# Kernel optimization log

Hardware: AMD Instinct MI355X
Metric: run time of the kernel (lower is better)

The kernel has to match this reference:

```python
import jax, jax.numpy as jnp
import numpy as np

# Swin block config (matches init_kwargs)
DIM = 192
HEADS = 6
HEAD_DIM = 32
INNER = HEADS * HEAD_DIM  # 192
MLP = 768
WS = 7                    # window size
DISP = WS // 2            # cyclic shift displacement = 3
NEG = -1e9                # stands in for -inf in the shift masks
EPS = 1e-5


def setup_inputs() -> dict:
    key = jax.random.key(0)
    ks = jax.random.split(key, 8)
    B, H, W = 8, 112, 112
    x = jax.random.normal(ks[0], (B, H, W, DIM), dtype=jnp.float32)
    w_qkv = jax.random.normal(ks[1], (DIM, 3 * INNER), dtype=jnp.float32) * 0.02
    w_out = jax.random.normal(ks[2], (INNER, DIM), dtype=jnp.float32) * 0.02
    b_out = jnp.zeros((DIM,), jnp.float32)
    pos_emb = jax.random.normal(ks[3], (2 * WS - 1, 2 * WS - 1), dtype=jnp.float32)
    ln1_g = jnp.ones((DIM,), jnp.float32)
    ln1_b = jnp.zeros((DIM,), jnp.float32)
    ln2_g = jnp.ones((DIM,), jnp.float32)
    ln2_b = jnp.zeros((DIM,), jnp.float32)
    w1 = jax.random.normal(ks[4], (DIM, MLP), dtype=jnp.float32) * 0.02
    b1 = jnp.zeros((MLP,), jnp.float32)
    w2 = jax.random.normal(ks[5], (MLP, DIM), dtype=jnp.float32) * 0.02
    b2 = jnp.zeros((DIM,), jnp.float32)
    return {"x": x, "w_qkv": w_qkv, "w_out": w_out, "b_out": b_out,
            "pos_emb": pos_emb, "ln1_g": ln1_g, "ln1_b": ln1_b,
            "ln2_g": ln2_g, "ln2_b": ln2_b,
            "w1": w1, "b1": b1, "w2": w2, "b2": b2}


def _layernorm(x, g, b):
    mu = jnp.mean(x, axis=-1, keepdims=True)
    var = jnp.var(x, axis=-1, keepdims=True)
    return (x - mu) * jax.lax.rsqrt(var + EPS) * g + b


def _rel_bias(pos_emb):
    # relative position bias, gathered to (ws^2, ws^2)
    coords = jnp.stack(jnp.meshgrid(jnp.arange(WS), jnp.arange(WS), indexing="ij"), -1).reshape(-1, 2)
    rel = coords[:, None, :] - coords[None, :, :] + WS - 1  # in [0, 2*WS-2]
    return pos_emb[rel[..., 0], rel[..., 1]]


def _shift_masks(nw_h, nw_w):
    ws2 = WS * WS
    ul = jnp.zeros((ws2, ws2), jnp.float32)
    ul = ul.at[-DISP * WS:, :-DISP * WS].set(NEG)
    ul = ul.at[:-DISP * WS, -DISP * WS:].set(NEG)
    lr = jnp.zeros((WS, WS, WS, WS), jnp.float32)
    lr = lr.at[:, -DISP:, :, :-DISP].set(NEG)
    lr = lr.at[:, :-DISP:, :, -DISP:].set(NEG)
    lr = lr.reshape(ws2, ws2)
    full = jnp.zeros((nw_h * nw_w, ws2, ws2), jnp.float32)
    full = full.at[-nw_w:].add(ul)            # bottom row of windows
    full = full.at[nw_w - 1::nw_w].add(lr)    # rightmost column of windows
    return full


def _window_attention(x, w_qkv, w_out, b_out, pos_emb):
    x = jnp.roll(x, (-DISP, -DISP), axis=(1, 2))  # cyclic shift
    B, H, W, _ = x.shape
    nw_h, nw_w = H // WS, W // WS
    ws2 = WS * WS
    qkv = x @ w_qkv  # (B,H,W,3*INNER)
    qkv = qkv.reshape(B, nw_h, WS, nw_w, WS, 3, HEADS, HEAD_DIM)
    # -> (3, B, heads, n_windows, ws^2, head_dim)
    qkv = qkv.transpose(5, 0, 6, 1, 3, 2, 4, 7).reshape(3, B, HEADS, nw_h * nw_w, ws2, HEAD_DIM)
    q, k, v = qkv[0], qkv[1], qkv[2]
    dots = jnp.einsum("bhwid,bhwjd->bhwij", q, k) * (HEAD_DIM ** -0.5)
    dots = dots + _rel_bias(pos_emb)                       # (ws2,ws2) broadcast
    dots = dots + _shift_masks(nw_h, nw_w)                 # (nw,ws2,ws2) broadcast
    attn = jax.nn.softmax(dots, axis=-1)
    out = jnp.einsum("bhwij,bhwjd->bhwid", attn, v)
    # merge windows back: (B, nw_h, WS, nw_w, WS, heads*head_dim)
    out = out.reshape(B, HEADS, nw_h, nw_w, WS, WS, HEAD_DIM)
    out = out.transpose(0, 2, 4, 3, 5, 1, 6).reshape(B, H, W, INNER)
    out = out @ w_out + b_out
    return jnp.roll(out, (DISP, DISP), axis=(1, 2))  # cyclic back-shift


def reference(x, w_qkv, w_out, b_out, pos_emb, ln1_g, ln1_b, ln2_g, ln2_b, w1, b1, w2, b2):
    # Residual(PreNorm(WindowAttention))
    x = x + _window_attention(_layernorm(x, ln1_g, ln1_b), w_qkv, w_out, b_out, pos_emb)
    # Residual(PreNorm(FeedForward))  with exact (erf) GELU as in nn.GELU
    h = _layernorm(x, ln2_g, ln2_b)
    h = jax.nn.gelu(h @ w1 + b1, approximate=False) @ w2 + b2
    return x + h
```

## Files before the change

kernel.cpp:

```cpp
#include <hip/hip_runtime.h>
#include <hip/hip_bf16.h>
#include <math.h>

typedef __hip_bfloat16 bf16;
typedef unsigned short ushort_t;
typedef __bf16 bf16x8 __attribute__((ext_vector_type(8)));
typedef unsigned short ushortx8 __attribute__((ext_vector_type(8)));
typedef float  f32x4  __attribute__((ext_vector_type(4)));

#define BATCH 8
#define HH 112
#define WW 112
#define CDIM 192
#define HEADS 6
#define HD 32
#define QKVW 576
#define MLPW 768
#define WS 7
#define WS2 49
#define NWH 16
#define NWW 16
#define NWIN 256
#define NTOK (BATCH*HH*WW)
#define NEGV (-1e9f)

typedef __attribute__((address_space(3))) void lds_void;
typedef const __attribute__((address_space(1))) void gbl_void;

__device__ __forceinline__ float toF(float v) { return v; }
__device__ __forceinline__ float toF(bf16 v) { return __bfloat162float(v); }
__device__ __forceinline__ bf16  f2b(float v) { return __float2bfloat16(v); }
__device__ __forceinline__ ushort_t f2u(float v) { bf16 b = __float2bfloat16(v); return *(ushort_t*)&b; }

__device__ __forceinline__ bool probe_is_bf16(const void* p) {
    const unsigned int* w = (const unsigned int*)p;
    int nz = 0, band = 0;
    #pragma unroll
    for (int i = 0; i < 16; i++) {
        unsigned int v = w[i];
        if (v == 0u) continue;
        nz++;
        unsigned int lo = v & 0xFFFFu, hi = v >> 16;
        unsigned int elo = (lo >> 7) & 0xFFu, ehi = (hi >> 7) & 0xFFu;
        bool okl = (lo != 0u) && (elo >= 0x60u) && (elo <= 0x9Fu);
        bool okh = (hi != 0u) && (ehi >= 0x60u) && (ehi <= 0x9Fu);
        if (okl && okh) band++;
    }
    return (nz == 0) || (band == nz);
}

__device__ __forceinline__ float read_any(const void* p, size_t i, bool isb) {
    return isb ? toF(((const bf16*)p)[i]) : ((const float*)p)[i];
}

__device__ __forceinline__ float wave_sum(float v) {
    #pragma unroll
    for (int o = 1; o < 64; o <<= 1) v += __shfl_xor(v, o, 64);
    return v;
}

__global__ void canon_kernel(const void* __restrict__ src, float* __restrict__ dst, int n) {
    bool isb = probe_is_bf16(src);
    int i = blockIdx.x * 256 + threadIdx.x;
    if (i < n) dst[i] = read_any(src, i, isb);
}

__global__ void canon_bt_kernel(const void* __restrict__ src, ushort_t* __restrict__ dstT,
                                int K, int N) {
    bool isb = probe_is_bf16(src);
    int i = blockIdx.x * 256 + threadIdx.x;
    if (i < K * N) {
        int k = i / N, n = i % N;
        dstT[(size_t)n * K + k] = f2u(read_any(src, i, isb));
    }
}

__global__ void ln1_kernel(const void* __restrict__ xraw, const float* __restrict__ g,
                           const float* __restrict__ bta, bf16* __restrict__ out) {
    bool xb = probe_is_bf16(xraw);
    int wave = threadIdx.x >> 6, lane = threadIdx.x & 63;
    int t = blockIdx.x * 4 + wave;
    size_t base = (size_t)t * CDIM;
    float v[3];
    #pragma unroll
    for (int i = 0; i < 3; i++) v[i] = read_any(xraw, base + lane + 64 * i, xb);
    float s  = v[0] + v[1] + v[2];
    float s2 = v[0]*v[0] + v[1]*v[1] + v[2]*v[2];
    s = wave_sum(s); s2 = wave_sum(s2);
    float mu = s * (1.0f / CDIM);
    float var = s2 * (1.0f / CDIM) - mu * mu;
    float rs = rsqrtf(var + 1e-5f);
    #pragma unroll
    for (int i = 0; i < 3; i++) {
        int c = lane + 64 * i;
        out[base + c] = f2b((v[i] - mu) * rs * g[c] + bta[c]);
    }
}

template <int EPI, int NY>
__global__ __launch_bounds__(256) void gemm_kernel(
    const ushort_t* __restrict__ A, const ushort_t* __restrict__ BT,
    const int K, const int N,
    const float* __restrict__ bias,
    const void* __restrict__ res,
    void* __restrict__ out)
{
    __shared__ ushort_t As[2][128 * 64];
    __shared__ ushort_t Bs[2][64 * 64];
    int tid = threadIdx.x;
    int per = gridDim.x >> 3;
    int sid = blockIdx.x;
    int w = (sid & 7) * per + (sid >> 3);
    int t0 = (w / NY) * 128;
    int n0 = (w % NY) * 64;
    int lane = tid & 63, wv = tid >> 6;
    int l15 = lane & 15, quad = lane >> 4;
    int lr = lane >> 3;
    int lc = lane & 7;

    f32x4 acc[2][4];
    #pragma unroll
    for (int i = 0; i < 2; i++)
        #pragma unroll
        for (int j = 0; j < 4; j++)
            acc[i][j] = (f32x4){0.f, 0.f, 0.f, 0.f};

    auto stage = [&](int kb, int buf) {
        #pragma unroll
        for (int it = 0; it < 4; it++) {
            int r = wv * 32 + it * 8 + lr;
            const ushort_t* src = &A[(size_t)(t0 + r) * K + kb + ((lc ^ (r & 7)) << 3)];
            __builtin_amdgcn_global_load_lds(
                (gbl_void*)src, (lds_void*)&As[buf][(wv * 32 + it * 8) * 64], 16, 0, 0);
        }
        #pragma unroll
        for (int it = 0; it < 2; it++) {
            int r = wv * 16 + it * 8 + lr;
            const ushort_t* src = &BT[(size_t)(n0 + r) * K + kb + ((lc ^ (r & 7)) << 3)];
            __builtin_amdgcn_global_load_lds(
                (gbl_void*)src, (lds_void*)&Bs[buf][(wv * 16 + it * 8) * 64], 16, 0, 0);
        }
    };

    const int nkb = K >> 6;
    stage(0, 0);
    __syncthreads();

    for (int t = 0; t < nkb; t++) {
        int cur = t & 1;
        if (t + 1 < nkb) stage((t + 1) << 6, cur ^ 1);
        #pragma unroll
        for (int kk = 0; kk < 64; kk += 32) {
            int cs = (((kk >> 3) + quad) ^ (l15 & 7)) << 3;
            bf16x8 af[2], bfr[4];
            #pragma unroll
            for (int i = 0; i < 2; i++)
                af[i] = *(const bf16x8*)(&As[cur][(wv * 32 + i * 16 + l15) * 64 + cs]);
            #pragma unroll
            for (int j = 0; j < 4; j++)
                bfr[j] = *(const bf16x8*)(&Bs[cur][(j * 16 + l15) * 64 + cs]);
            #pragma unroll
            for (int i = 0; i < 2; i++)
                #pragma unroll
                for (int j = 0; j < 4; j++)
                    acc[i][j] = __builtin_amdgcn_mfma_f32_16x16x32_bf16(af[i], bfr[j], acc[i][j], 0, 0, 0);
        }
        __syncthreads();
    }

    bool xb = false;
    if (EPI == 1) xb = probe_is_bf16(res);

    #pragma unroll
    for (int i = 0; i < 2; i++) {
        #pragma unroll
        for (int j = 0; j < 4; j++) {
            #pragma unroll
            for (int r = 0; r < 4; r++) {
                int row = wv * 32 + i * 16 + quad * 4 + r;
                int col = n0 + j * 16 + l15;
                size_t t = (size_t)(t0 + row);
                float v = acc[i][j][r];
                if (EPI == 0) {
                    ((bf16*)out)[t * N + col] = f2b(v);
                } else {
                    size_t o = t * CDIM + col;
                    ((bf16*)out)[o] = f2b(v + bias[col] + read_any(res, o, xb));
                }
            }
        }
    }
}

__global__ __launch_bounds__(256, 2) void fused_mlp_kernel(
    const bf16* __restrict__ X,
    const ushort_t* __restrict__ W1T,
    const ushort_t* __restrict__ W2T,
    const float* __restrict__ g, const float* __restrict__ bta,
    const float* __restrict__ b1, const float* __restrict__ b2,
    float* __restrict__ out)
{
    __shared__ ushort_t W1s[3 * 64 * 64];
    __shared__ ushort_t W2s[192 * 64];
    __shared__ ushort_t Hs[128 * 64];
    int tid = threadIdx.x;
    int lane = tid & 63, wv = tid >> 6;
    int l15 = lane & 15, quad = lane >> 4;
    int lr = lane >> 3, lc = lane & 7;
    int t0 = blockIdx.x * 128;

    auto stageW1 = [&](int c) {
        #pragma unroll
        for (int p = 0; p < 3; p++)
            #pragma unroll
            for (int rg = 0; rg < 2; rg++) {
                int rowb = wv * 16 + rg * 8;
                const ushort_t* src =
                    &W1T[(size_t)(c * 64 + rowb + lr) * CDIM + p * 64 + ((lc ^ lr) << 3)];
                __builtin_amdgcn_global_load_lds(
                    (gbl_void*)src, (lds_void*)&W1s[p * 4096 + rowb * 64], 16, 0, 0);
            }
    };
    auto stageW2 = [&](int c) {
        #pragma unroll
        for (int rg = 0; rg < 6; rg++) {
            int rowb = wv * 48 + rg * 8;
            const ushort_t* src =
                &W2T[(size_t)(rowb + lr) * MLPW + c * 64 + ((lc ^ lr) << 3)];
            __builtin_amdgcn_global_load_lds(
                (gbl_void*)src, (lds_void*)&W2s[rowb * 64], 16, 0, 0);
        }
    };

    stageW1(0);
    stageW2(0);

    bf16x8 af[2][6];
    float s[2] = {0.f, 0.f}, s2[2] = {0.f, 0.f};
    #pragma unroll
    for (int m = 0; m < 2; m++) {
        size_t rb = (size_t)(t0 + wv * 32 + m * 16 + l15) * CDIM;
        #pragma unroll
        for (int kk = 0; kk < 6; kk++) {
            af[m][kk] = *(const bf16x8*)((const ushort_t*)X + rb + kk * 32 + quad * 8);
            #pragma unroll
            for (int j = 0; j < 8; j++) {
                float f = (float)af[m][kk][j];
                s[m] += f; s2[m] += f * f;
            }
        }
    }
    #pragma unroll
    for (int m = 0; m < 2; m++) {
        s[m]  += __shfl_xor(s[m], 16, 64);  s[m]  += __shfl_xor(s[m], 32, 64);
        s2[m] += __shfl_xor(s2[m], 16, 64); s2[m] += __shfl_xor(s2[m], 32, 64);
    }
    #pragma unroll
    for (int kk = 0; kk < 6; kk++) {
        int c0 = kk * 32 + quad * 8;
        float4 g0 = *(const float4*)(g + c0), g1 = *(const float4*)(g + c0 + 4);
        float4 b0 = *(const float4*)(bta + c0), b1v = *(const float4*)(bta + c0 + 4);
        const float* gp[2] = {&g0.x, &g1.x};
        const float* bp[2] = {&b0.x, &b1v.x};
        #pragma unroll
        for (int m = 0; m < 2; m++) {
            float mu = s[m] * (1.0f / CDIM);
            float var = s2[m] * (1.0f / CDIM) - mu * mu;
            float rs = rsqrtf(var + 1e-5f);
            #pragma unroll
            for (int j = 0; j < 8; j++)
                af[m][kk][j] = (__bf16)(((float)af[m][kk][j] - mu) * rs * gp[j >> 2][j & 3]
                                        + bp[j >> 2][j & 3]);
        }
    }

    f32x4 acc2[2][12];
    #pragma unroll
    for (int m = 0; m < 2; m++)
        #pragma unroll
        for (int nt = 0; nt < 12; nt++) acc2[m][nt] = (f32x4){0.f, 0.f, 0.f, 0.f};

    __syncthreads();

    for (int c = 0; c < 12; c++) {
        f32x4 hacc[2][4];
        #pragma unroll
        for (int m = 0; m < 2; m++)
            #pragma unroll
            for (int nt = 0; nt < 4; nt++) hacc[m][nt] = (f32x4){0.f, 0.f, 0.f, 0.f};
        #pragma unroll
        for (int kk = 0; kk < 6; kk++) {
            int p = kk >> 1;
            int cc = (kk & 1) * 4 + quad;
            #pragma unroll
            for (int nt = 0; nt < 4; nt++) {
                int n = nt * 16 + l15;
                bf16x8 bfr = *(const bf16x8*)(&W1s[p * 4096 + n * 64 + ((cc ^ (n & 7)) << 3)]);
                #pragma unroll
                for (int m = 0; m < 2; m++)
                    hacc[m][nt] = __builtin_amdgcn_mfma_f32_16x16x32_bf16(af[m][kk], bfr, hacc[m][nt], 0, 0, 0);
            }
        }
        float b1v[4];
        #pragma unroll
        for (int nt = 0; nt < 4; nt++) b1v[nt] = b1[c * 64 + nt * 16 + l15];
        #pragma unroll
        for (int m = 0; m < 2; m++) {
            #pragma unroll
            for (int nt = 0; nt < 4; nt++) {
                #pragma unroll
                for (int r = 0; r < 4; r++) {
                    int i = wv * 32 + m * 16 + quad * 4 + r;
                    int hcol = nt * 16 + l15;
                    float a = hacc[m][nt][r] + b1v[nt];
                    float gl = 0.5f * a * (1.0f + erff(a * 0.70710678118654752f));
                    Hs[i * 64 + (((hcol >> 3) ^ (i & 7)) << 3) + (hcol & 7)] = f2u(gl);
                }
            }
        }
        __syncthreads();

        if (c + 1 < 12) stageW1(c + 1);

        #pragma unroll
        for (int kt = 0; kt < 2; kt++) {
            int cc = kt * 4 + quad;
            bf16x8 pa[2];
            #pragma unroll
            for (int m = 0; m < 2; m++) {
                int row = wv * 32 + m * 16 + l15;
                pa[m] = *(const bf16x8*)(&Hs[row * 64 + ((cc ^ (row & 7)) << 3)]);
            }
            #pragma unroll
            for (int nt = 0; nt < 12; nt++) {
                int n = nt * 16 + l15;
                bf16x8 wb = *(const bf16x8*)(&W2s[n * 64 + ((cc ^ (n & 7)) << 3)]);
                #pragma unroll
                for (int m = 0; m < 2; m++)
                    acc2[m][nt] = __builtin_amdgcn_mfma_f32_16x16x32_bf16(pa[m], wb, acc2[m][nt], 0, 0, 0);
            }
        }
        __syncthreads();

        if (c + 1 < 12) stageW2(c + 1);
    }

    #pragma unroll
    for (int nt = 0; nt < 12; nt++) {
        float bb = b2[nt * 16 + l15];
        #pragma unroll
        for (int m = 0; m < 2; m++) {
            #pragma unroll
            for (int r = 0; r < 4; r++) {
                int row = t0 + wv * 32 + m * 16 + quad * 4 + r;
                int col = nt * 16 + l15;
                size_t o = (size_t)row * CDIM + col;
                out[o] = acc2[m][nt][r] + bb + toF(X[o]);
            }
        }
    }
}

__global__ __launch_bounds__(256) void attn_kernel(const bf16* __restrict__ qkv,
                                                   const float* __restrict__ pos_emb,
                                                   bf16* __restrict__ y) {
    __shared__ ushort_t Ps[4][64 * 72];
    __shared__ ushort_t Vt[4][32 * 72];
    __shared__ float pe[169];

    int tid = threadIdx.x;
    int wv = tid >> 6, lane = tid & 63;
    int l15 = lane & 15, quad = lane >> 4;

    int per = gridDim.x >> 3;
    int sid = blockIdx.x;
    int bid = (sid & 7) * per + (sid >> 3);
    int gid = bid * 4 + wv;
    int h = gid % HEADS;
    int rest = gid / HEADS;
    int win = rest % NWIN;
    int b = rest / NWIN;
    int wi = win >> 4, wj = win & 15;

    for (int i = lane; i < 169; i += 64) pe[i] = pos_emb[i];
    __syncthreads();

    auto tok = [&](int i) -> int {
        i = min(i, 48);
        int pi = (i * 37) >> 8;
        int pj = i - pi * 7;
        int ui = wi * WS + pi + 3; if (ui >= HH) ui -= HH;
        int uj = wj * WS + pj + 3; if (uj >= WW) uj -= WW;
        return (b * HH + ui) * WW + uj;
    };

    bf16x8 qf[4], kf[4];
    #pragma unroll
    for (int t = 0; t < 4; t++) {
        size_t base = (size_t)tok(t * 16 + l15) * QKVW + h * HD + quad * 8;
        qf[t] = *(const bf16x8*)(qkv + base);
        kf[t] = *(const bf16x8*)(qkv + base + CDIM);
    }

    #pragma unroll
    for (int it = 0; it < 4; it++) {
        int idx = lane + it * 64;
        int p = idx >> 2, dc = idx & 3;
        size_t base = (size_t)tok(p) * QKVW + 2 * CDIM + h * HD + dc * 8;
        ushortx8 v = *(const ushortx8*)((const ushort_t*)qkv + base);
        #pragma unroll
        for (int jj = 0; jj < 8; jj++)
            Vt[wv][(dc * 8 + jj) * 72 + p] = v[jj];
    }

    f32x4 acc[4][4];
    #pragma unroll
    for (int mt = 0; mt < 4; mt++)
        #pragma unroll
        for (int nt = 0; nt < 4; nt++)
            acc[mt][nt] = (f32x4){0.f, 0.f, 0.f, 0.f};
    #pragma unroll
    for (int mt = 0; mt < 4; mt++)
        #pragma unroll
        for (int nt = 0; nt < 4; nt++)
            acc[mt][nt] = __builtin_amdgcn_mfma_f32_16x16x32_bf16(qf[mt], kf[nt], acc[mt][nt], 0, 0, 0);

    bool m_ul = (wi == NWH - 1);
    bool m_lr = (wj == NWW - 1);
    int kpi[4], kpj[4];
    bool jval[4];
    #pragma unroll
    for (int nt = 0; nt < 4; nt++) {
        int j = nt * 16 + l15;
        jval[nt] = (j < WS2);
        int jc = min(j, 48);
        kpi[nt] = (jc * 37) >> 8;
        kpj[nt] = jc - kpi[nt] * 7;
    }
    #pragma unroll
    for (int mt = 0; mt < 4; mt++) {
        #pragma unroll
        for (int r = 0; r < 4; r++) {
            int i = mt * 16 + quad * 4 + r;
            int ic = min(i, 48);
            int pi = (ic * 37) >> 8;
            int pj = ic - pi * 7;
            #pragma unroll
            for (int nt = 0; nt < 4; nt++) {
                float s = acc[mt][nt][r] * 0.17677669529663689f
                        + pe[(pi - kpi[nt] + 6) * 13 + (pj - kpj[nt] + 6)];
                if (m_ul && ((pi >= 4) != (kpi[nt] >= 4))) s += NEGV;
                if (m_lr && ((pj >= 4) != (kpj[nt] >= 4))) s += NEGV;
                if (!jval[nt]) s = NEGV;
                acc[mt][nt][r] = s;
            }
            float mx = fmaxf(fmaxf(acc[mt][0][r], acc[mt][1][r]),
                             fmaxf(acc[mt][2][r], acc[mt][3][r]));
            #pragma unroll
            for (int o = 1; o < 16; o <<= 1) mx = fmaxf(mx, __shfl_xor(mx, o, 64));
            float sum = 0.f;
            #pragma unroll
            for (int nt = 0; nt < 4; nt++) {
                float e = __expf(acc[mt][nt][r] - mx);
                acc[mt][nt][r] = e;
                sum += e;
            }
            #pragma unroll
            for (int o = 1; o < 16; o <<= 1) sum += __shfl_xor(sum, o, 64);
            float inv = 1.0f / sum;
            #pragma unroll
            for (int nt = 0; nt < 4; nt++) acc[mt][nt][r] *= inv;
        }
    }

    #pragma unroll
    for (int mt = 0; mt < 4; mt++)
        #pragma unroll
        for (int nt = 0; nt < 4; nt++)
            #pragma unroll
            for (int r = 0; r < 4; r++)
                Ps[wv][(mt * 16 + quad * 4 + r) * 72 + nt * 16 + l15] = f2u(acc[mt][nt][r]);

    f32x4 oacc[4][2];
    #pragma unroll
    for (int mt = 0; mt < 4; mt++)
        #pragma unroll
        for (int nt = 0; nt < 2; nt++)
            oacc[mt][nt] = (f32x4){0.f, 0.f, 0.f, 0.f};
    #pragma unroll
    for (int kt = 0; kt < 2; kt++) {
        bf16x8 pa[4], vb[2];
        #pragma unroll
        for (int mt = 0; mt < 4; mt++)
            pa[mt] = *(const bf16x8*)(&Ps[wv][(mt * 16 + l15) * 72 + kt * 32 + quad * 8]);
        #pragma unroll
        for (int nt = 0; nt < 2; nt++)
            vb[nt] = *(const bf16x8*)(&Vt[wv][(nt * 16 + l15) * 72 + kt * 32 + quad * 8]);
        #pragma unroll
        for (int mt = 0; mt < 4; mt++)
            #pragma unroll
            for (int nt = 0; nt < 2; nt++)
                oacc[mt][nt] = __builtin_amdgcn_mfma_f32_16x16x32_bf16(pa[mt], vb[nt], oacc[mt][nt], 0, 0, 0);
    }

    #pragma unroll
    for (int mt = 0; mt < 4; mt++) {
        #pragma unroll
        for (int r = 0; r < 4; r++) {
            int i = mt * 16 + quad * 4 + r;
            if (i < WS2) {
                size_t base = (size_t)tok(i) * CDIM + h * HD + l15;
                #pragma unroll
                for (int nt = 0; nt < 2; nt++)
                    y[base + nt * 16] = f2b(oacc[mt][nt][r]);
            }
        }
    }
}

extern "C" void kernel_launch(void* const* d_in, const int* in_sizes, int n_in,
                              void* d_out, int out_size, void* d_ws, size_t ws_size,
                              hipStream_t stream) {
    float* out = (float*)d_out;

    size_t szA = (size_t)NTOK * CDIM * sizeof(bf16);
    size_t szQ = (size_t)NTOK * QKVW * sizeof(bf16);
    size_t szY = (size_t)NTOK * CDIM * sizeof(bf16);
    size_t szX = (size_t)NTOK * CDIM * sizeof(bf16);
    size_t szP = 3072 * sizeof(float);
    size_t szT = 442368 * sizeof(ushort_t);
    if (ws_size < szA + szQ + szY + szX + szP + szT) return;
    bf16*     bufA = (bf16*)d_ws;
    bf16*     bufQ = (bf16*)((char*)d_ws + szA);
    bf16*     bufY = (bf16*)((char*)d_ws + szA + szQ);
    bf16*     bufX = (bf16*)((char*)d_ws + szA + szQ + szY);
    float*    cW   = (float*)((char*)d_ws + szA + szQ + szY + szX);
    ushort_t* cT   = (ushort_t*)((char*)d_ws + szA + szQ + szY + szX + szP);

    float* cBout = cW + 0;
    float* cPe   = cW + 192;
    float* cL1g  = cW + 384;
    float* cL1b  = cW + 576;
    float* cL2g  = cW + 768;
    float* cL2b  = cW + 960;
    float* cB1   = cW + 1152;
    float* cB2   = cW + 1920;

    ushort_t* tWqkv = cT + 0;
    ushort_t* tWout = cT + 110592;
    ushort_t* tW1   = cT + 147456;
    ushort_t* tW2   = cT + 294912;

    dim3 b256(256);
    #define CANON(src, dst, n) canon_kernel<<<((n)+255)/256, b256, 0, stream>>>((src), (dst), (n))
    CANON(d_in[3],  cBout, 192);
    CANON(d_in[4],  cPe,   169);
    CANON(d_in[5],  cL1g,  192);
    CANON(d_in[6],  cL1b,  192);
    CANON(d_in[7],  cL2g,  192);
    CANON(d_in[8],  cL2b,  192);
    CANON(d_in[10], cB1,   768);
    CANON(d_in[12], cB2,   192);
    #undef CANON
    #define CANONT(src, dst, K, N) \
        canon_bt_kernel<<<((K)*(N)+255)/256, b256, 0, stream>>>((src), (dst), (K), (N))
    CANONT(d_in[1],  tWqkv, CDIM, QKVW);
    CANONT(d_in[2],  tWout, CDIM, CDIM);
    CANONT(d_in[9],  tW1,   CDIM, MLPW);
    CANONT(d_in[11], tW2,   MLPW, CDIM);
    #undef CANONT

    int gLN = NTOK / 4;
    int gM  = NTOK / 128;
    int gAT = BATCH * NWIN * HEADS / 4;
    int gF  = NTOK / 128;

    ln1_kernel<<<gLN, b256, 0, stream>>>(d_in[0], cL1g, cL1b, bufA);
    gemm_kernel<0, 9><<<gM * 9, b256, 0, stream>>>(
        (const ushort_t*)bufA, tWqkv, CDIM, QKVW, nullptr, nullptr, bufQ);
    attn_kernel<<<gAT, b256, 0, stream>>>(bufQ, cPe, bufY);
    gemm_kernel<1, 3><<<gM * 3, b256, 0, stream>>>(
        (const ushort_t*)bufY, tWout, CDIM, CDIM, cBout, d_in[0], bufX);
    fused_mlp_kernel<<<gF, b256, 0, stream>>>(
        bufX, tW1, tW2, cL2g, cL2b, cB1, cB2, out);
}
```

Before: 536.2 us.

## Stage full K=192 in GEMM and widen fused MLP to 256-token blocks

The projection GEMMs now specialise for K=192: all three 64-wide K slices of A and B are loaded into LDS up front, with a single barrier before a fully unrolled MFMA loop. This replaces the double-buffered K loop and its per-iteration barriers. The fused MLP kernel moves to 512 threads handling 256 tokens per block, so each staged weight chunk is shared by twice as many tokens. The larger Hs buffer and the (512,4) launch bound tighten LDS and register budgets, which risks spills or lower occupancy.

Result: slower. 834.0 us (+55.5%).

```diff
diff --git a/kernel.cpp b/kernel.cpp
--- a/kernel.cpp
+++ b/kernel.cpp
@@ -98,15 +98,15 @@
 }
 
 template <int EPI, int NY>
-__global__ __launch_bounds__(256) void gemm_kernel(
+__global__ __launch_bounds__(256) void gemm192_kernel(
     const ushort_t* __restrict__ A, const ushort_t* __restrict__ BT,
-    const int K, const int N,
+    const int N,
     const float* __restrict__ bias,
     const void* __restrict__ res,
     void* __restrict__ out)
 {
-    __shared__ ushort_t As[2][128 * 64];
-    __shared__ ushort_t Bs[2][64 * 64];
+    __shared__ ushort_t As[3][128 * 64];
+    __shared__ ushort_t Bs[3][64 * 64];
     int tid = threadIdx.x;
     int per = gridDim.x >> 3;
     int sid = blockIdx.x;
@@ -115,8 +115,25 @@
     int n0 = (w % NY) * 64;
     int lane = tid & 63, wv = tid >> 6;
     int l15 = lane & 15, quad = lane >> 4;
-    int lr = lane >> 3;
-    int lc = lane & 7;
+    int lr = lane >> 3, lc = lane & 7;
+
+    #pragma unroll
+    for (int p = 0; p < 3; p++) {
+        #pragma unroll
+        for (int it = 0; it < 4; it++) {
+            int r = wv * 32 + it * 8 + lr;
+            const ushort_t* src = &A[(size_t)(t0 + r) * 192 + p * 64 + ((lc ^ lr) << 3)];
+            __builtin_amdgcn_global_load_lds(
+                (gbl_void*)src, (lds_void*)&As[p][(wv * 32 + it * 8) * 64], 16, 0, 0);
+        }
+        #pragma unroll
+        for (int it = 0; it < 2; it++) {
+            int r = wv * 16 + it * 8 + lr;
+            const ushort_t* src = &BT[(size_t)(n0 + r) * 192 + p * 64 + ((lc ^ lr) << 3)];
+            __builtin_amdgcn_global_load_lds(
+                (gbl_void*)src, (lds_void*)&Bs[p][(wv * 16 + it * 8) * 64], 16, 0, 0);
+        }
+    }
 
     f32x4 acc[2][4];
     #pragma unroll
@@ -125,47 +142,24 @@
         for (int j = 0; j < 4; j++)
             acc[i][j] = (f32x4){0.f, 0.f, 0.f, 0.f};
 
-    auto stage = [&](int kb, int buf) {
-        #pragma unroll
-        for (int it = 0; it < 4; it++) {
-            int r = wv * 32 + it * 8 + lr;
-            const ushort_t* src = &A[(size_t)(t0 + r) * K + kb + ((lc ^ (r & 7)) << 3)];
-            __builtin_amdgcn_global_load_lds(
-                (gbl_void*)src, (lds_void*)&As[buf][(wv * 32 + it * 8) * 64], 16, 0, 0);
-        }
-        #pragma unroll
-        for (int it = 0; it < 2; it++) {
-            int r = wv * 16 + it * 8 + lr;
-            const ushort_t* src = &BT[(size_t)(n0 + r) * K + kb + ((lc ^ (r & 7)) << 3)];
-            __builtin_amdgcn_global_load_lds(
-                (gbl_void*)src, (lds_void*)&Bs[buf][(wv * 16 + it * 8) * 64], 16, 0, 0);
-        }
-    };
-
-    const int nkb = K >> 6;
-    stage(0, 0);
     __syncthreads();
 
-    for (int t = 0; t < nkb; t++) {
-        int cur = t & 1;
-        if (t + 1 < nkb) stage((t + 1) << 6, cur ^ 1);
-        #pragma unroll
-        for (int kk = 0; kk < 64; kk += 32) {
-            int cs = (((kk >> 3) + quad) ^ (l15 & 7)) << 3;
-            bf16x8 af[2], bfr[4];
-            #pragma unroll
-            for (int i = 0; i < 2; i++)
-                af[i] = *(const bf16x8*)(&As[cur][(wv * 32 + i * 16 + l15) * 64 + cs]);
+    #pragma unroll
+    for (int kk = 0; kk < 6; kk++) {
+        int p = kk >> 1;
+        int cs = ((((kk & 1) * 4 + quad)) ^ (l15 & 7)) << 3;
+        bf16x8 af[2], bfr[4];
+        #pragma unroll
+        for (int i = 0; i < 2; i++)
+            af[i] = *(const bf16x8*)(&As[p][(wv * 32 + i * 16 + l15) * 64 + cs]);
+        #pragma unroll
+        for (int j = 0; j < 4; j++)
+            bfr[j] = *(const bf16x8*)(&Bs[p][(j * 16 + l15) * 64 + cs]);
+        #pragma unroll
+        for (int i = 0; i < 2; i++)
             #pragma unroll
             for (int j = 0; j < 4; j++)
-                bfr[j] = *(const bf16x8*)(&Bs[cur][(j * 16 + l15) * 64 + cs]);
-            #pragma unroll
-            for (int i = 0; i < 2; i++)
-                #pragma unroll
-                for (int j = 0; j < 4; j++)
-                    acc[i][j] = __builtin_amdgcn_mfma_f32_16x16x32_bf16(af[i], bfr[j], acc[i][j], 0, 0, 0);
-        }
-        __syncthreads();
+                acc[i][j] = __builtin_amdgcn_mfma_f32_16x16x32_bf16(af[i], bfr[j], acc[i][j], 0, 0, 0);
     }
 
     bool xb = false;
@@ -192,7 +186,7 @@
     }
 }
 
-__global__ __launch_bounds__(256, 2) void fused_mlp_kernel(
+__global__ __launch_bounds__(512, 4) void fused_mlp_kernel(
     const bf16* __restrict__ X,
     const ushort_t* __restrict__ W1T,
     const ushort_t* __restrict__ W2T,
@@ -202,29 +196,26 @@
 {
     __shared__ ushort_t W1s[3 * 64 * 64];
     __shared__ ushort_t W2s[192 * 64];
-    __shared__ ushort_t Hs[128 * 64];
+    __shared__ ushort_t Hs[256 * 64];
     int tid = threadIdx.x;
     int lane = tid & 63, wv = tid >> 6;
     int l15 = lane & 15, quad = lane >> 4;
     int lr = lane >> 3, lc = lane & 7;
-    int t0 = blockIdx.x * 128;
+    int t0 = blockIdx.x * 256;
 
     auto stageW1 = [&](int c) {
         #pragma unroll
-        for (int p = 0; p < 3; p++)
-            #pragma unroll
-            for (int rg = 0; rg < 2; rg++) {
-                int rowb = wv * 16 + rg * 8;
-                const ushort_t* src =
-                    &W1T[(size_t)(c * 64 + rowb + lr) * CDIM + p * 64 + ((lc ^ lr) << 3)];
-                __builtin_amdgcn_global_load_lds(
-                    (gbl_void*)src, (lds_void*)&W1s[p * 4096 + rowb * 64], 16, 0, 0);
-            }
+        for (int p = 0; p < 3; p++) {
+            const ushort_t* src =
+                &W1T[(size_t)(c * 64 + wv * 8 + lr) * CDIM + p * 64 + ((lc ^ lr) << 3)];
+            __builtin_amdgcn_global_load_lds(
+                (gbl_void*)src, (lds_void*)&W1s[p * 4096 + (wv * 8) * 64], 16, 0, 0);
+        }
     };
     auto stageW2 = [&](int c) {
         #pragma unroll
-        for (int rg = 0; rg < 6; rg++) {
-            int rowb = wv * 48 + rg * 8;
+        for (int rg = 0; rg < 3; rg++) {
+            int rowb = wv * 24 + rg * 8;
             const ushort_t* src =
                 &W2T[(size_t)(rowb + lr) * MLPW + c * 64 + ((lc ^ lr) << 3)];
             __builtin_amdgcn_global_load_lds(
@@ -551,7 +542,7 @@
     ushort_t* tW1   = cT + 147456;
     ushort_t* tW2   = cT + 294912;
 
-    dim3 b256(256);
+    dim3 b256(256), b512(512);
     #define CANON(src, dst, n) canon_kernel<<<((n)+255)/256, b256, 0, stream>>>((src), (dst), (n))
     CANON(d_in[3],  cBout, 192);
     CANON(d_in[4],  cPe,   169);
@@ -573,14 +564,14 @@
     int gLN = NTOK / 4;
     int gM  = NTOK / 128;
     int gAT = BATCH * NWIN * HEADS / 4;
-    int gF  = NTOK / 128;
+    int gF  = NTOK / 256;
 
     ln1_kernel<<<gLN, b256, 0, stream>>>(d_in[0], cL1g, cL1b, bufA);
-    gemm_kernel<0, 9><<<gM * 9, b256, 0, stream>>>(
-        (const ushort_t*)bufA, tWqkv, CDIM, QKVW, nullptr, nullptr, bufQ);
+    gemm192_kernel<0, 9><<<gM * 9, b256, 0, stream>>>(
+        (const ushort_t*)bufA, tWqkv, QKVW, nullptr, nullptr, bufQ);
     attn_kernel<<<gAT, b256, 0, stream>>>(bufQ, cPe, bufY);
-    gemm_kernel<1, 3><<<gM * 3, b256, 0, stream>>>(
-        (const ushort_t*)bufY, tWout, CDIM, CDIM, cBout, d_in[0], bufX);
-    fused_mlp_kernel<<<gF, b256, 0, stream>>>(
+    gemm192_kernel<1, 3><<<gM * 3, b256, 0, stream>>>(
+        (const ushort_t*)bufY, tWout, CDIM, cBout, d_in[0], bufX);
+    fused_mlp_kernel<<<gF, b512, 0, stream>>>(
         bufX, tW1, tW2, cL2g, cL2b, cB1, cB2, out);
 }
```
